# Kernel tuning notes

Hardware: AMD Instinct MI355X
Metric: run time of the kernel (lower is better)

Reference implementation:

```python
import jax, jax.numpy as jnp
import numpy as np

ATT_HEAD = 12
IN_DIM = 768
OUT_DIM = IN_DIM // ATT_HEAD
LEAKY_ALPHA = 0.2
B, N = 8, 512


def setup_inputs() -> dict:
    key = jax.random.key(0)
    ks = jax.random.split(key, 8)
    feat_in = jax.random.normal(ks[0], (B, N, IN_DIM), dtype=jnp.float32)
    adj = jax.random.randint(ks[1], (B, N, N), 0, 2) > 0
    # xavier_uniform for W: fan_in=in_dim, fan_out=out_dim
    lim_W = float(np.sqrt(6.0 / (IN_DIM + OUT_DIM)))
    W = jax.random.uniform(ks[2], (ATT_HEAD, IN_DIM, OUT_DIM), minval=-lim_W, maxval=lim_W, dtype=jnp.float32)
    b = jnp.zeros((OUT_DIM,), dtype=jnp.float32)
    lim_w = float(np.sqrt(6.0 / (OUT_DIM + 1)))
    w_src = jax.random.uniform(ks[3], (ATT_HEAD, OUT_DIM, 1), minval=-lim_w, maxval=lim_w, dtype=jnp.float32)
    w_dst = jax.random.uniform(ks[4], (ATT_HEAD, OUT_DIM, 1), minval=-lim_w, maxval=lim_w, dtype=jnp.float32)
    # xavier_normal for H.weight [in_dim, in_dim]
    std_H = float(np.sqrt(2.0 / (IN_DIM + IN_DIM)))
    H_w = jax.random.normal(ks[5], (IN_DIM, IN_DIM), dtype=jnp.float32) * std_H
    H_b = jax.random.normal(ks[6], (IN_DIM,), dtype=jnp.float32) * 0.01
    return {"feat_in": feat_in, "adj": adj, "W": W, "b": b,
            "w_src": w_src, "w_dst": w_dst, "H_w": H_w, "H_b": H_b}


def reference(feat_in, adj, W, b, w_src, w_dst, H_w, H_b):
    # h: [B, heads, N, out_dim]
    h = jnp.einsum('bnd,ade->bane', feat_in, W)
    th = jnp.tanh(h)
    attn_src = jnp.einsum('bane,aeo->bano', th, w_src)  # [B,A,N,1]
    attn_dst = jnp.einsum('bane,aeo->bano', th, w_dst)  # [B,A,N,1]
    attn = attn_src + jnp.swapaxes(attn_dst, 2, 3)      # [B,A,N,N]
    attn = jnp.where(attn >= 0, attn, LEAKY_ALPHA * attn)
    mask = ~adj[:, None, :, :]                           # [B,1,N,N]
    attn = jnp.where(mask, jnp.float32(-999.0), attn)
    attn = jax.nn.softmax(attn, axis=-1)
    feat_out = jnp.einsum('banm,bame->bane', attn, h) + b
    feat_out = jnp.swapaxes(feat_out, 1, 2).reshape(feat_in.shape[0], feat_in.shape[1], -1)
    feat_out = jax.nn.elu(feat_out)
    gate = jax.nn.sigmoid(feat_in @ H_w.T + H_b)
    return gate * feat_out + (1.0 - gate) * feat_in
```

## Files before the change

### kernel.cpp

```cpp
#include <hip/hip_runtime.h>
#include <hip/hip_bf16.h>

#define BB 8
#define NN 512
#define AH 12
#define DIN 768
#define EE 64
#define MM (BB*NN)
#define YY (BB*AH)
#define LEAKY 0.2f

typedef unsigned short u16;
typedef unsigned int u32;
typedef __attribute__((ext_vector_type(8))) short short8;
typedef __attribute__((ext_vector_type(4))) float f32x4;
typedef __attribute__((ext_vector_type(4))) u32 u32x4;
typedef __attribute__((ext_vector_type(4))) u16 u16x4;

static __device__ __forceinline__ u16 f2bf(float f) {
    u32 u = __builtin_bit_cast(u32, f);
    u32 r = (u + 0x7FFFu + ((u >> 16) & 1u)) >> 16;
    return (u16)r;
}
static __device__ __forceinline__ u32 pk2(float a, float b) {
    return (u32)f2bf(a) | ((u32)f2bf(b) << 16);
}
static __device__ __forceinline__ u32 cvtpk(float a, float b) {
    u32 r;
    asm("v_cvt_pk_bf16_f32 %0, %1, %2" : "=v"(r) : "v"(a), "v"(b));
    return r;
}
static __device__ __forceinline__ float ftanh(float x) {
    x = fminf(fmaxf(x, -15.f), 15.f);
    return 1.f - 2.f / (__expf(2.f * x) + 1.f);
}
static __device__ __forceinline__ float sigm(float z) {
    z = fminf(fmaxf(z, -80.f), 80.f);
    return 1.f / (1.f + __expf(-z));
}
static __device__ __forceinline__ void gl_lds16(const u16* g, u16* l) {
    __builtin_amdgcn_global_load_lds((const __attribute__((address_space(1))) unsigned int*)g,
                                     (__attribute__((address_space(3))) unsigned int*)l,
                                     16, 0, 0);
}

static __device__ __forceinline__ void mfma_probe(int lane, int* prow, int* pcol) {
    int q = lane >> 4, x = lane & 15;
    short8 af, bf;
#pragma unroll
    for (int j = 0; j < 8; j++) {
        int k = q * 8 + j;
        af[j] = (short)f2bf((k < 16) ? (float)(x * 16 + k) : 0.f);
        bf[j] = (short)f2bf((k == x) ? 1.f : 0.f);
    }
    f32x4 d = {};
    d = __builtin_amdgcn_mfma_f32_16x16x32_bf16(af, bf, d, 0, 0, 0);
#pragma unroll
    for (int r = 0; r < 4; r++) {
        int v = (int)(d[r] + 0.5f);
        prow[r] = v >> 4;
        pcol[r] = v & 15;
    }
}

#define N_FEAT (MM*DIN)
#define N_W    (AH*DIN*EE)
#define PACK_BLOCKS (MM/4)
#define FEATV_BLOCKS (N_FEAT/1024)
#define HWBV_BLOCKS (N_W/1024)
#define WT_BLOCKS (AH*(DIN/64))
#define PREP_BLOCKS (PACK_BLOCKS + FEATV_BLOCKS + HWBV_BLOCKS + WT_BLOCKS)

__global__ __launch_bounds__(256) void prep_kernel(const int* __restrict__ adj,
                                                   const float* __restrict__ feat,
                                                   const float* __restrict__ W,
                                                   const float* __restrict__ Hw,
                                                   u32* __restrict__ maskbuf,
                                                   u16* __restrict__ featb,
                                                   u16* __restrict__ Wt,
                                                   u16* __restrict__ Hwb) {
    int blk = blockIdx.x, t = threadIdx.x;
    if (blk < PACK_BLOCKS) {
        int w = t >> 6, ln = t & 63;
        int row = blk * 4 + w;
        const int* ar = adj + (size_t)row * NN;
#pragma unroll
        for (int it = 0; it < 8; it++) {
            unsigned long long bal = __ballot(ar[it * 64 + ln] != 0);
            if (ln == 0) {
                maskbuf[row * 16 + it * 2]     = (u32)bal;
                maskbuf[row * 16 + it * 2 + 1] = (u32)(bal >> 32);
            }
        }
        return;
    }
    blk -= PACK_BLOCKS;
    if (blk < FEATV_BLOCKS) {
        int i = blk * 1024 + t * 4;
        float4 v = *(const float4*)&feat[i];
        u16x4 o = { f2bf(v.x), f2bf(v.y), f2bf(v.z), f2bf(v.w) };
        *(u16x4*)&featb[i] = o;
        return;
    }
    blk -= FEATV_BLOCKS;
    if (blk < HWBV_BLOCKS) {
        int i = blk * 1024 + t * 4;
        float4 v = *(const float4*)&Hw[i];
        u16x4 o = { f2bf(v.x), f2bf(v.y), f2bf(v.z), f2bf(v.w) };
        *(u16x4*)&Hwb[i] = o;
        return;
    }
    blk -= HWBV_BLOCKS;
    __shared__ float tile[64][65];
    int a = blk / (DIN / 64), d0 = (blk % (DIN / 64)) * 64;
    int rl = t >> 4, c4 = (t & 15) * 4;
#pragma unroll
    for (int i = 0; i < 4; i++) {
        int dl = i * 16 + rl;
        float4 v = *(const float4*)&W[((size_t)a * DIN + d0 + dl) * EE + c4];
        tile[dl][c4 + 0] = v.x;
        tile[dl][c4 + 1] = v.y;
        tile[dl][c4 + 2] = v.z;
        tile[dl][c4 + 3] = v.w;
    }
    __syncthreads();
#pragma unroll
    for (int i = 0; i < 4; i++) {
        int e = i * 16 + rl;
        u16x4 o = { f2bf(tile[c4 + 0][e]), f2bf(tile[c4 + 1][e]),
                    f2bf(tile[c4 + 2][e]), f2bf(tile[c4 + 3][e]) };
        *(u16x4*)&Wt[(size_t)a * EE * DIN + (size_t)e * DIN + d0 + c4] = o;
    }
}

__global__ __launch_bounds__(256) void gemm_fused_kernel(const u16* __restrict__ featb,
                                                         const u16* __restrict__ Wt,
                                                         const u16* __restrict__ Hwb,
                                                         const float* __restrict__ wsrc,
                                                         const float* __restrict__ wdst,
                                                         const float* __restrict__ Hb,
                                                         u16* __restrict__ hT,
                                                         float2* __restrict__ Spair,
                                                         float2* __restrict__ Dpair,
                                                         float* __restrict__ Gbuf) {
    __shared__ u16 As[64 * 64];
    __shared__ u16 BsW[64 * 64];
    __shared__ u16 BsG[64 * 64];
    __shared__ alignas(16) float cs[64][68];
    int t = threadIdx.x, w = t >> 6, lane = t & 63, q = lane >> 4, x = lane & 15;
    int m0 = blockIdx.x * 64, a = blockIdx.y;

    int wm = w & 1, wn = w >> 1, xr = x & 7;
    int srow = t >> 3;
    int skoff = ((t & 7) ^ (srow & 7)) * 8;
    const u16* Agp  = featb + (size_t)m0 * DIN + srow * DIN + skoff;
    const u16* BWgp = Wt + (size_t)a * EE * DIN + srow * DIN + skoff;
    const u16* BGgp = Hwb + (size_t)(a * EE) * DIN + srow * DIN + skoff;
    u16* Asw  = As  + w * 512;
    u16* BWsw = BsW + w * 512;
    u16* BGsw = BsG + w * 512;
    const u16* ApA  = As  + (wm * 32 + x) * 64;
    const u16* ApBW = BsW + (wn * 32 + x) * 64;
    const u16* ApBG = BsG + (wn * 32 + x) * 64;
    f32x4 aW00 = {}, aW01 = {}, aW10 = {}, aW11 = {};
    f32x4 aG00 = {}, aG01 = {}, aG10 = {}, aG11 = {};

    for (int k0 = 0; k0 < DIN; k0 += 64) {
        gl_lds16(Agp + k0, Asw);
        gl_lds16(Agp + 32 * DIN + k0, Asw + 2048);
        gl_lds16(BWgp + k0, BWsw);
        gl_lds16(BWgp + 32 * DIN + k0, BWsw + 2048);
        gl_lds16(BGgp + k0, BGsw);
        gl_lds16(BGgp + 32 * DIN + k0, BGsw + 2048);
        __syncthreads();
#pragma unroll
        for (int kk = 0; kk < 2; kk++) {
            int c8 = ((q + kk * 4) ^ xr) * 8;
            short8 a0 = *(const short8*)(ApA + c8);
            short8 a1 = *(const short8*)(ApA + 16 * 64 + c8);
            short8 bW0 = *(const short8*)(ApBW + c8);
            short8 bW1 = *(const short8*)(ApBW + 16 * 64 + c8);
            short8 bG0 = *(const short8*)(ApBG + c8);
            short8 bG1 = *(const short8*)(ApBG + 16 * 64 + c8);
            aW00 = __builtin_amdgcn_mfma_f32_16x16x32_bf16(a0, bW0, aW00, 0, 0, 0);
            aW01 = __builtin_amdgcn_mfma_f32_16x16x32_bf16(a0, bW1, aW01, 0, 0, 0);
            aW10 = __builtin_amdgcn_mfma_f32_16x16x32_bf16(a1, bW0, aW10, 0, 0, 0);
            aW11 = __builtin_amdgcn_mfma_f32_16x16x32_bf16(a1, bW1, aW11, 0, 0, 0);
            aG00 = __builtin_amdgcn_mfma_f32_16x16x32_bf16(a0, bG0, aG00, 0, 0, 0);
            aG01 = __builtin_amdgcn_mfma_f32_16x16x32_bf16(a0, bG1, aG01, 0, 0, 0);
            aG10 = __builtin_amdgcn_mfma_f32_16x16x32_bf16(a1, bG0, aG10, 0, 0, 0);
            aG11 = __builtin_amdgcn_mfma_f32_16x16x32_bf16(a1, bG1, aG11, 0, 0, 0);
        }
        __syncthreads();
    }

    int prow[4], pcol[4];
    mfma_probe(lane, prow, pcol);

#pragma unroll
    for (int r = 0; r < 4; r++) {
        cs[wm * 32 + prow[r]][wn * 32 + pcol[r]]           = aW00[r];
        cs[wm * 32 + prow[r]][wn * 32 + 16 + pcol[r]]      = aW01[r];
        cs[wm * 32 + 16 + prow[r]][wn * 32 + pcol[r]]      = aW10[r];
        cs[wm * 32 + 16 + prow[r]][wn * 32 + 16 + pcol[r]] = aW11[r];
    }
    __syncthreads();

    int b = m0 >> 9;
    int y = b * AH + a;
    int nbase = m0 & 511;
    {
        int kcb = nbase >> 3;
#pragma unroll
        for (int i = 0; i < 2; i++) {
            int idx = i * 256 + t;
            int kcl = idx >> 6, e = idx & 63;
            int r0 = kcl * 8;
            u32x4 wv = { pk2(cs[r0 + 0][e], cs[r0 + 1][e]),
                         pk2(cs[r0 + 2][e], cs[r0 + 3][e]),
                         pk2(cs[r0 + 4][e], cs[r0 + 5][e]),
                         pk2(cs[r0 + 6][e], cs[r0 + 7][e]) };
            *(u32x4*)&hT[((((size_t)y << 6) + kcb + kcl) << 6 | e) * 8] = wv;
        }
    }
    {
        int r = t >> 2, cg = t & 3;
        float s = 0.f, d = 0.f;
#pragma unroll
        for (int i = 0; i < 16; i++) {
            int e2 = cg * 16 + i;
            float th = ftanh(cs[r][e2]);
            s += th * wsrc[a * EE + e2];
            d += th * wdst[a * EE + e2];
        }
        s += __shfl_xor(s, 1); s += __shfl_xor(s, 2);
        d += __shfl_xor(d, 1); d += __shfl_xor(d, 2);
        if (cg == 0) {
            s = fminf(fmaxf(s, -40.f), 40.f);
            d = fminf(fmaxf(d, -40.f), 40.f);
            Spair[y * NN + nbase + r] = make_float2(__expf(s), __expf(0.2f * s));
            Dpair[y * NN + nbase + r] = make_float2(__expf(d), __expf(0.2f * d));
        }
    }
    __syncthreads();

#pragma unroll
    for (int r = 0; r < 4; r++) {
        cs[wm * 32 + prow[r]][wn * 32 + pcol[r]]           = aG00[r];
        cs[wm * 32 + prow[r]][wn * 32 + 16 + pcol[r]]      = aG01[r];
        cs[wm * 32 + 16 + prow[r]][wn * 32 + pcol[r]]      = aG10[r];
        cs[wm * 32 + 16 + prow[r]][wn * 32 + 16 + pcol[r]] = aG11[r];
    }
    __syncthreads();

    {
        int n0 = a * EE;
        float4 hb = *(const float4*)&Hb[n0 + (t & 15) * 4];
#pragma unroll
        for (int p = 0; p < 4; p++) {
            int ml = p * 16 + (t >> 4), c4 = (t & 15) * 4;
            float4 v4 = *(const float4*)&cs[ml][c4];
            size_t idx = (size_t)(m0 + ml) * DIN + n0 + c4;
            float4 o;
            o.x = sigm(v4.x + hb.x);
            o.y = sigm(v4.y + hb.y);
            o.z = sigm(v4.z + hb.z);
            o.w = sigm(v4.w + hb.w);
            *(float4*)&Gbuf[idx] = o;
        }
    }
}

__global__ __launch_bounds__(256) void attn_kernel(const u16* __restrict__ hT,
                                                   const float2* __restrict__ Spair,
                                                   const float2* __restrict__ Dpair,
                                                   const u32* __restrict__ maskbuf,
                                                   const float* __restrict__ bias,
                                                   const float* __restrict__ Gbuf,
                                                   const float* __restrict__ feat,
                                                   float* __restrict__ out) {
    __shared__ alignas(16) float2 sd2[NN];
    __shared__ u32 smask[64][17];
    __shared__ float silv[64];
    __shared__ alignas(16) float cs[64][68];

    int t = threadIdx.x;
    int y = blockIdx.y, bb = y / AH, a = y % AH;
    int i0 = blockIdx.x * 64;
    int w = t >> 6, lane = t & 63, q = lane >> 4, x = lane & 15;

    sd2[t] = Dpair[y * NN + t];
    sd2[t + 256] = Dpair[y * NN + 256 + t];
#pragma unroll
    for (int p = 0; p < 4; p++) {
        int idx = p * 256 + t, r = idx >> 4, c = idx & 15;
        smask[r][c] = maskbuf[((bb << 9) + i0 + r) * 16 + c];
    }
    __syncthreads();

    int rowl = w * 16 + x;
    float2 se = Spair[y * NN + i0 + rowl];
    float es1 = se.x, es2 = se.y;

    u32 anym = 0;
#pragma unroll
    for (int c = 0; c < 16; c++) anym |= smask[rowl][c];
    int uni = (anym == 0);

    const u16* hTy = hT + ((size_t)y << 12) * 8;
    f32x4 acc[4] = {};
    float lsum = 0.f;

#pragma unroll 2
    for (int k0 = 0; k0 < NN; k0 += 32) {
        u32 mb = smask[rowl][k0 >> 5] >> (q * 8);
        const float4* sdp = (const float4*)&sd2[k0 + q * 8];
        float pv[8];
#pragma unroll
        for (int jj = 0; jj < 4; jj++) {
            float4 d4 = sdp[jj];
            float p0 = fmaxf(es1 * d4.x, es2 * d4.y);
            float p1 = fmaxf(es1 * d4.z, es2 * d4.w);
            p0 = ((mb >> (2 * jj)) & 1) ? p0 : 0.f;
            p1 = ((mb >> (2 * jj + 1)) & 1) ? p1 : 0.f;
            p0 = uni ? 1.0f : p0;
            p1 = uni ? 1.0f : p1;
            lsum += p0 + p1;
            pv[2 * jj] = p0;
            pv[2 * jj + 1] = p1;
        }
        short8 af = __builtin_bit_cast(short8, (u32x4){
            cvtpk(pv[0], pv[1]), cvtpk(pv[2], pv[3]),
            cvtpk(pv[4], pv[5]), cvtpk(pv[6], pv[7])});
        const u16* hp = hTy + ((((k0 >> 3) + q) << 6) + x) * 8;
        short8 b0 = *(const short8*)(hp);
        short8 b1 = *(const short8*)(hp + 16 * 8);
        short8 b2 = *(const short8*)(hp + 32 * 8);
        short8 b3 = *(const short8*)(hp + 48 * 8);
        acc[0] = __builtin_amdgcn_mfma_f32_16x16x32_bf16(af, b0, acc[0], 0, 0, 0);
        acc[1] = __builtin_amdgcn_mfma_f32_16x16x32_bf16(af, b1, acc[1], 0, 0, 0);
        acc[2] = __builtin_amdgcn_mfma_f32_16x16x32_bf16(af, b2, acc[2], 0, 0, 0);
        acc[3] = __builtin_amdgcn_mfma_f32_16x16x32_bf16(af, b3, acc[3], 0, 0, 0);
    }

    lsum += __shfl_xor(lsum, 16);
    lsum += __shfl_xor(lsum, 32);
    if (q == 0) silv[rowl] = 1.f / fmaxf(lsum, 1e-30f);

    int prow[4], pcol[4];
    mfma_probe(lane, prow, pcol);
#pragma unroll
    for (int nt = 0; nt < 4; nt++)
#pragma unroll
        for (int r = 0; r < 4; r++)
            cs[w * 16 + prow[r]][nt * 16 + pcol[r]] = acc[nt][r];
    __syncthreads();

    float4 b4 = *(const float4*)&bias[(t & 15) * 4];
#pragma unroll
    for (int p = 0; p < 4; p++) {
        int nl = p * 16 + (t >> 4), e4 = (t & 15) * 4;
        float il = silv[nl];
        float4 c4 = *(const float4*)&cs[nl][e4];
        size_t base = ((size_t)(bb << 9) + i0 + nl) * DIN + a * EE + e4;
        float4 g4 = *(const float4*)&Gbuf[base];
        float4 f4 = *(const float4*)&feat[base];
        float4 o;
        float v, e;
        v = c4.x * il + b4.x; e = v > 0.f ? v : __expf(v) - 1.f; o.x = g4.x * e + (1.f - g4.x) * f4.x;
        v = c4.y * il + b4.y; e = v > 0.f ? v : __expf(v) - 1.f; o.y = g4.y * e + (1.f - g4.y) * f4.y;
        v = c4.z * il + b4.z; e = v > 0.f ? v : __expf(v) - 1.f; o.z = g4.z * e + (1.f - g4.z) * f4.z;
        v = c4.w * il + b4.w; e = v > 0.f ? v : __expf(v) - 1.f; o.w = g4.w * e + (1.f - g4.w) * f4.w;
        *(float4*)&out[base] = o;
    }
}

extern "C" void kernel_launch(void* const* d_in, const int* in_sizes, int n_in,
                              void* d_out, int out_size, void* d_ws, size_t ws_size,
                              hipStream_t stream) {
    const float* feat  = (const float*)d_in[0];
    const int*   adj   = (const int*)  d_in[1];
    const float* W     = (const float*)d_in[2];
    const float* bvec  = (const float*)d_in[3];
    const float* wsrc  = (const float*)d_in[4];
    const float* wdst  = (const float*)d_in[5];
    const float* Hw    = (const float*)d_in[6];
    const float* Hb    = (const float*)d_in[7];
    float* out = (float*)d_out;

    char* ws = (char*)d_ws;
    u16*    featb   = (u16*)(ws);
    u16*    Wt      = (u16*)(ws + 6291456);
    u16*    Hwb     = (u16*)(ws + 7471104);
    u16*    hT      = (u16*)(ws + 8650752);
    float2* Spair   = (float2*)(ws + 14942208);
    float2* Dpair   = (float2*)(ws + 15335424);
    u32*    maskbuf = (u32*)(ws + 15728640);
    float*  Gbuf    = (float*)(ws + 15990784);

    prep_kernel<<<PREP_BLOCKS, 256, 0, stream>>>(
        adj, feat, W, Hw, maskbuf, featb, Wt, Hwb);
    gemm_fused_kernel<<<dim3(MM / 64, AH), 256, 0, stream>>>(
        featb, Wt, Hwb, wsrc, wdst, Hb, hT, Spair, Dpair, Gbuf);
    attn_kernel<<<dim3(NN / 64, YY), 256, 0, stream>>>(
        hT, Spair, Dpair, maskbuf, bvec, Gbuf, feat, out);
}
```

Measured before the change: 120.9 us.

## Double-buffer LDS tiles in fused projection GEMM to overlap loads with MFMA

Splits shared memory into two sets of A/W/H tiles and prefetches the next K-slice via global-to-LDS loads while MFMAs run on the current slice. This is meant to hide global load latency behind compute and removes one barrier per iteration. The epilogue's cs buffer now aliases the first tile buffers, and LDS use rises to 48KB, which may reduce occupancy. Correctness relies on the async LDS loads being complete at the barrier.

```diff
diff --git a/kernel.cpp b/kernel.cpp
--- a/kernel.cpp
+++ b/kernel.cpp
@@ -143,10 +143,15 @@
                                                          float2* __restrict__ Spair,
                                                          float2* __restrict__ Dpair,
                                                          float* __restrict__ Gbuf) {
-    __shared__ u16 As[64 * 64];
-    __shared__ u16 BsW[64 * 64];
-    __shared__ u16 BsG[64 * 64];
-    __shared__ alignas(16) float cs[64][68];
+    __shared__ alignas(16) char smem[49152];
+    u16* As0 = (u16*)smem;
+    u16* BW0 = (u16*)(smem + 8192);
+    u16* BG0 = (u16*)(smem + 16384);
+    u16* As1 = (u16*)(smem + 24576);
+    u16* BW1 = (u16*)(smem + 32768);
+    u16* BG1 = (u16*)(smem + 40960);
+    float (*cs)[68] = (float (*)[68])smem;
+
     int t = threadIdx.x, w = t >> 6, lane = t & 63, q = lane >> 4, x = lane & 15;
     int m0 = blockIdx.x * 64, a = blockIdx.y;
 
@@ -156,43 +161,58 @@
     const u16* Agp  = featb + (size_t)m0 * DIN + srow * DIN + skoff;
     const u16* BWgp = Wt + (size_t)a * EE * DIN + srow * DIN + skoff;
     const u16* BGgp = Hwb + (size_t)(a * EE) * DIN + srow * DIN + skoff;
-    u16* Asw  = As  + w * 512;
-    u16* BWsw = BsW + w * 512;
-    u16* BGsw = BsG + w * 512;
-    const u16* ApA  = As  + (wm * 32 + x) * 64;
-    const u16* ApBW = BsW + (wn * 32 + x) * 64;
-    const u16* ApBG = BsG + (wn * 32 + x) * 64;
+    int wo = w * 512;
     f32x4 aW00 = {}, aW01 = {}, aW10 = {}, aW11 = {};
     f32x4 aG00 = {}, aG01 = {}, aG10 = {}, aG11 = {};
 
-    for (int k0 = 0; k0 < DIN; k0 += 64) {
-        gl_lds16(Agp + k0, Asw);
-        gl_lds16(Agp + 32 * DIN + k0, Asw + 2048);
-        gl_lds16(BWgp + k0, BWsw);
-        gl_lds16(BWgp + 32 * DIN + k0, BWsw + 2048);
-        gl_lds16(BGgp + k0, BGsw);
-        gl_lds16(BGgp + 32 * DIN + k0, BGsw + 2048);
+#define STAGE(A_, BW_, BG_, K_)                                   \
+    do {                                                          \
+        gl_lds16(Agp + (K_), (A_) + wo);                          \
+        gl_lds16(Agp + 32 * DIN + (K_), (A_) + wo + 2048);        \
+        gl_lds16(BWgp + (K_), (BW_) + wo);                        \
+        gl_lds16(BWgp + 32 * DIN + (K_), (BW_) + wo + 2048);      \
+        gl_lds16(BGgp + (K_), (BG_) + wo);                        \
+        gl_lds16(BGgp + 32 * DIN + (K_), (BG_) + wo + 2048);      \
+    } while (0)
+
+#define COMPUTE(A_, BW_, BG_)                                                       \
+    do {                                                                            \
+        const u16* ApA  = (A_)  + (wm * 32 + x) * 64;                               \
+        const u16* ApBW = (BW_) + (wn * 32 + x) * 64;                               \
+        const u16* ApBG = (BG_) + (wn * 32 + x) * 64;                               \
+        _Pragma("unroll")                                                           \
+        for (int kk = 0; kk < 2; kk++) {                                            \
+            int c8 = ((q + kk * 4) ^ xr) * 8;                                       \
+            short8 a0 = *(const short8*)(ApA + c8);                                 \
+            short8 a1 = *(const short8*)(ApA + 16 * 64 + c8);                       \
+            short8 bW0 = *(const short8*)(ApBW + c8);                               \
+            short8 bW1 = *(const short8*)(ApBW + 16 * 64 + c8);                     \
+            short8 bG0 = *(const short8*)(ApBG + c8);                               \
+            short8 bG1 = *(const short8*)(ApBG + 16 * 64 + c8);                     \
+            aW00 = __builtin_amdgcn_mfma_f32_16x16x32_bf16(a0, bW0, aW00, 0, 0, 0); \
+            aW01 = __builtin_amdgcn_mfma_f32_16x16x32_bf16(a0, bW1, aW01, 0, 0, 0); \
+            aW10 = __builtin_amdgcn_mfma_f32_16x16x32_bf16(a1, bW0, aW10, 0, 0, 0); \
+            aW11 = __builtin_amdgcn_mfma_f32_16x16x32_bf16(a1, bW1, aW11, 0, 0, 0); \
+            aG00 = __builtin_amdgcn_mfma_f32_16x16x32_bf16(a0, bG0, aG00, 0, 0, 0); \
+            aG01 = __builtin_amdgcn_mfma_f32_16x16x32_bf16(a0, bG1, aG01, 0, 0, 0); \
+            aG10 = __builtin_amdgcn_mfma_f32_16x16x32_bf16(a1, bG0, aG10, 0, 0, 0); \
+            aG11 = __builtin_amdgcn_mfma_f32_16x16x32_bf16(a1, bG1, aG11, 0, 0, 0); \
+        }                                                                           \
+    } while (0)
+
+    STAGE(As0, BW0, BG0, 0);
+    __syncthreads();
+#pragma unroll 1
+    for (int k0 = 0; k0 < DIN; k0 += 128) {
+        STAGE(As1, BW1, BG1, k0 + 64);
+        COMPUTE(As0, BW0, BG0);
         __syncthreads();
-#pragma unroll
-        for (int kk = 0; kk < 2; kk++) {
-            int c8 = ((q + kk * 4) ^ xr) * 8;
-            short8 a0 = *(const short8*)(ApA + c8);
-            short8 a1 = *(const short8*)(ApA + 16 * 64 + c8);
-            short8 bW0 = *(const short8*)(ApBW + c8);
-            short8 bW1 = *(const short8*)(ApBW + 16 * 64 + c8);
-            short8 bG0 = *(const short8*)(ApBG + c8);
-            short8 bG1 = *(const short8*)(ApBG + 16 * 64 + c8);
-            aW00 = __builtin_amdgcn_mfma_f32_16x16x32_bf16(a0, bW0, aW00, 0, 0, 0);
-            aW01 = __builtin_amdgcn_mfma_f32_16x16x32_bf16(a0, bW1, aW01, 0, 0, 0);
-            aW10 = __builtin_amdgcn_mfma_f32_16x16x32_bf16(a1, bW0, aW10, 0, 0, 0);
-            aW11 = __builtin_amdgcn_mfma_f32_16x16x32_bf16(a1, bW1, aW11, 0, 0, 0);
-            aG00 = __builtin_amdgcn_mfma_f32_16x16x32_bf16(a0, bG0, aG00, 0, 0, 0);
-            aG01 = __builtin_amdgcn_mfma_f32_16x16x32_bf16(a0, bG1, aG01, 0, 0, 0);
-            aG10 = __builtin_amdgcn_mfma_f32_16x16x32_bf16(a1, bG0, aG10, 0, 0, 0);
-            aG11 = __builtin_amdgcn_mfma_f32_16x16x32_bf16(a1, bG1, aG11, 0, 0, 0);
-        }
+        if (k0 + 128 < DIN) STAGE(As0, BW0, BG0, k0 + 128);
+        COMPUTE(As1, BW1, BG1);
         __syncthreads();
     }
+#undef STAGE
+#undef COMPUTE
 
     int prow[4], pcol[4];
     mfma_probe(lane, prow, pcol);
```

Measured after the change: 118.3 us. -2.1%, faster.
